# Kernel optimization log

Measured on AMD Instinct MI355X. Metric: run time of the kernel, lower is better.

## Reference

```python
import jax, jax.numpy as jnp
import numpy as np

B, S, D, H = 4, 2048, 1024, 16
HD = D // H
THETA = 10000.0


def rope(x, pos, theta=THETA):
    # x: [..., seq, d], pos: broadcastable to [..., seq]
    d = x.shape[-1]
    half = d // 2
    inv_freq = 1.0 / (theta ** (jnp.arange(half, dtype=jnp.float32) * 2.0 / d))  # [half]
    ang = pos[..., None].astype(jnp.float32) * inv_freq  # [..., seq, half]
    cos, sin = jnp.cos(ang), jnp.sin(ang)
    x1, x2 = x[..., 0::2], x[..., 1::2]
    r1 = x1 * cos - x2 * sin
    r2 = x1 * sin + x2 * cos
    return jnp.stack([r1, r2], axis=-1).reshape(x.shape).astype(x.dtype)


def setup_inputs() -> dict:
    key = jax.random.key(0)
    ks = jax.random.split(key, 5)
    x = jax.random.normal(ks[0], (B, S, D), dtype=jnp.float32)
    token_positions = jnp.tile(jnp.arange(S, dtype=jnp.int64 if jax.config.jax_enable_x64 else jnp.int32), (B, 1))
    scale = 0.02
    Wq = jax.random.normal(ks[1], (D, D), dtype=jnp.float32) * scale
    Wk = jax.random.normal(ks[2], (D, D), dtype=jnp.float32) * scale
    Wv = jax.random.normal(ks[3], (D, D), dtype=jnp.float32) * scale
    Wo = jax.random.normal(ks[4], (D, D), dtype=jnp.float32) * scale
    return {"x": x, "token_positions": token_positions, "Wq": Wq, "Wk": Wk, "Wv": Wv, "Wo": Wo}


def reference(x, token_positions, Wq, Wk, Wv, Wo):
    b, s, d = x.shape
    # QKV projections (torch Linear: x @ W.T), split heads -> [b, h, s, hd]
    def proj(W):
        y = jnp.einsum('bsd,ed->bse', x, W)
        return y.reshape(b, s, H, HD).transpose(0, 2, 1, 3)
    Q, K, V = proj(Wq), proj(Wk), proj(Wv)
    # token_positions [..., seq] -> [..., 1, seq] to broadcast over heads
    pos = token_positions[:, None, :]  # [b, 1, s]
    Q = rope(Q, pos)
    K = rope(K, pos)
    # causal mask and scaled dot-product attention
    idx = jnp.arange(s)
    causal = idx[:, None] >= idx[None, :]  # [s, s], query >= key
    scores = jnp.einsum('bhqd,bhkd->bhqk', Q, K) / jnp.sqrt(jnp.float32(HD))
    scores = jnp.where(causal, scores, -jnp.inf)
    weights = jax.nn.softmax(scores, axis=-1)
    o = jnp.einsum('bhqk,bhkd->bhqd', weights, V)
    o = o.transpose(0, 2, 1, 3).reshape(b, s, d)  # merge heads
    return jnp.einsum('bsd,ed->bse', o, Wo)
```

## Files before the change

### kernel.cpp

```cpp
#include <hip/hip_runtime.h>

#define S_LEN 2048
#define NH 16
#define HDIM 64
#define DMODEL 1024

typedef __attribute__((ext_vector_type(8))) short bf16x8;
typedef __attribute__((ext_vector_type(4))) float f32x4;

__device__ __forceinline__ short f2bf(float f) {
    union { float f; unsigned u; } x; x.f = f;
    unsigned r = x.u + 0x7fffu + ((x.u >> 16) & 1u);
    return (short)(r >> 16);
}

#define GLDS(g, l) __builtin_amdgcn_global_load_lds( \
    (__attribute__((address_space(1))) void*)(g),    \
    (__attribute__((address_space(3))) void*)(l), 16, 0, 0)

#define QSCALE 0.18033688011112042f
#define FREQ_L 0.41524101186109327f

__global__ __launch_bounds__(256) void prep(const float* __restrict__ x,
                                            const float* __restrict__ wq,
                                            const float* __restrict__ wk,
                                            const float* __restrict__ wv,
                                            const float* __restrict__ wo,
                                            const int* __restrict__ tp,
                                            short* __restrict__ xb,
                                            short* __restrict__ wqb,
                                            short* __restrict__ wkb,
                                            short* __restrict__ wvb,
                                            short* __restrict__ wob,
                                            float2* __restrict__ tab) {
    int bid = blockIdx.x;
    if (bid < 8192) {
        int i = bid * 256 + threadIdx.x;
        float4 v = ((const float4*)x)[i];
        short4 o;
        o.x = f2bf(v.x); o.y = f2bf(v.y); o.z = f2bf(v.z); o.w = f2bf(v.w);
        ((short4*)xb)[i] = o;
    } else if (bid < 12288) {
        int sel = (bid - 8192) >> 10;
        const float* in = sel == 0 ? wq : sel == 1 ? wk : sel == 2 ? wv : wo;
        short* out = sel == 0 ? wqb : sel == 1 ? wkb : sel == 2 ? wvb : wob;
        int i = ((bid - 8192) & 1023) * 256 + threadIdx.x;
        float4 v = ((const float4*)in)[i];
        short4 o;
        o.x = f2bf(v.x); o.y = f2bf(v.y); o.z = f2bf(v.z); o.w = f2bf(v.w);
        ((short4*)out)[i] = o;
    } else {
        int idx = (bid - 12288) * 256 + threadIdx.x;
        int b = idx >> 16, s = (idx >> 5) & 2047, i = idx & 31;
        float p = (float)tp[(b << 11) + s];
        float freq = exp2f(-(float)i * FREQ_L);
        float sn, cs;
        sincosf(p * freq, &sn, &cs);
        tab[idx] = make_float2(cs, sn);
    }
}

__global__ __launch_bounds__(256) void gemm_qkv(const short* __restrict__ A,
                                                const short* __restrict__ Bq,
                                                const short* __restrict__ Bk,
                                                const short* __restrict__ Bv,
                                                const float2* __restrict__ tab,
                                                short* __restrict__ Qo,
                                                short* __restrict__ Ko,
                                                short* __restrict__ Vo) {
    constexpr int K = 1024, BK = 64;
    __shared__ __align__(16) short smem[2 * 128 * BK];
    short* sa = smem;
    short* sb = smem + 128 * BK;

    const int sel = blockIdx.x >> 3;
    const int bn = blockIdx.x & 7;
    const int bm = blockIdx.y;
    const short* Bm = sel == 0 ? Bq : sel == 1 ? Bk : Bv;
    short* Cb = sel == 0 ? Qo : sel == 1 ? Ko : Vo;

    const int tid = threadIdx.x;
    const int lane = tid & 63;
    const int w = tid >> 6;
    const int wm = w >> 1, wn = w & 1;
    const int quad = lane >> 4, l16 = lane & 15;
    const int l7 = l16 & 7;

    int aoff[4], boff[4];
#pragma unroll
    for (int i = 0; i < 4; i++) {
        int Lc = i * 256 + tid;
        int row = Lc >> 3;
        int cc = (Lc & 7) ^ (row & 7);
        aoff[i] = (bm * 128 + row) * K + cc * 8;
        boff[i] = (bn * 128 + row) * K + cc * 8;
    }

    f32x4 acc[4][4] = {};

    for (int k0 = 0; k0 < K; k0 += BK) {
#pragma unroll
        for (int i = 0; i < 4; i++)
            GLDS(A + aoff[i] + k0, (char*)sa + i * 4096 + w * 1024);
#pragma unroll
        for (int i = 0; i < 4; i++)
            GLDS(Bm + boff[i] + k0, (char*)sb + i * 4096 + w * 1024);
        __syncthreads();

#pragma unroll
        for (int kc = 0; kc < 2; kc++) {
            const int c = ((kc * 4 + quad) ^ l7) * 8;
            bf16x8 af[4], bfm[4];
#pragma unroll
            for (int mi = 0; mi < 4; mi++)
                af[mi] = *(const bf16x8*)&sa[(wm * 64 + mi * 16 + l16) * BK + c];
#pragma unroll
            for (int ni = 0; ni < 4; ni++)
                bfm[ni] = *(const bf16x8*)&sb[(wn * 64 + ni * 16 + l16) * BK + c];
#pragma unroll
            for (int mi = 0; mi < 4; mi++)
#pragma unroll
                for (int ni = 0; ni < 4; ni++)
                    acc[mi][ni] = __builtin_amdgcn_mfma_f32_16x16x32_bf16(af[mi], bfm[ni],
                                                                          acc[mi][ni], 0, 0, 0);
        }
        __syncthreads();
    }

    const int gm0 = bm * 128 + wm * 64;
    const int gn0 = bn * 128 + wn * 64;

    if (sel == 2) {
        short* T = smem;
#pragma unroll
        for (int mi = 0; mi < 4; mi++) {
            int lmb = wm * 64 + mi * 16 + quad * 4;
#pragma unroll
            for (int ni = 0; ni < 4; ni++) {
                int ln = wn * 64 + ni * 16 + l16;
                short4 pk;
                pk.x = f2bf(acc[mi][ni][0]);
                pk.y = f2bf(acc[mi][ni][1]);
                pk.z = f2bf(acc[mi][ni][2]);
                pk.w = f2bf(acc[mi][ni][3]);
                *(short4*)&T[ln * 128 + (lmb ^ ((ln & 15) << 3))] = pk;
            }
        }
        __syncthreads();
        const int row = tid >> 1, half = tid & 1;
        const int grow = bn * 128 + row;
        const int gb = (bm * 128) >> 11;
        const int gs0 = (bm * 128) & 2047;
        short* dst = Cb + (((size_t)(gb * NH + (grow >> 6)) * HDIM + (grow & 63)) * S_LEN
                           + gs0 + half * 64);
#pragma unroll
        for (int j = 0; j < 8; j++) {
            bf16x8 v = *(const bf16x8*)&T[row * 128 +
                        ((half * 64 + j * 8) ^ ((row & 15) << 3))];
            *(bf16x8*)(dst + j * 8) = v;
        }
    } else {
        const float qs = (sel == 0) ? QSCALE : 1.0f;
#pragma unroll
        for (int mi = 0; mi < 4; mi++)
#pragma unroll
            for (int r = 0; r < 4; r++) {
                int gm = gm0 + mi * 16 + quad * 4 + r;
                const float2* trow = tab + (gm << 5);
                int b = gm >> 11, s = gm & 2047;
#pragma unroll
                for (int ni = 0; ni < 4; ni++) {
                    float2 cs = trow[ni * 8 + (l16 >> 1)];
                    float v = acc[mi][ni][r];
                    float prt = __shfl_xor(v, 1, 64);
                    float val = (l16 & 1) ? (prt * cs.y + v * cs.x)
                                          : (v * cs.x - prt * cs.y);
                    int gn = gn0 + ni * 16 + l16;
                    int h = gn >> 6, hd = gn & 63;
                    Cb[((b * NH + h) * S_LEN + s) * HDIM + hd] = f2bf(val * qs);
                }
            }
    }
}

__global__ __launch_bounds__(256) void gemm_o(const short* __restrict__ A,
                                              const short* __restrict__ Bw,
                                              float* __restrict__ Cf) {
    constexpr int N = 1024, K = 1024, BK = 32;
    __shared__ __align__(16) short sa[3][128 * BK];
    __shared__ __align__(16) short sb[3][64 * BK];

    const int tid = threadIdx.x;
    const int lane = tid & 63;
    const int w = tid >> 6;
    const int quad = lane >> 4, l16 = lane & 15;
    const int bn = blockIdx.x, bm = blockIdx.y;
    const int arow0 = bm * 128, brow0 = bn * 64;

    int aoff[2], boff;
#pragma unroll
    for (int i = 0; i < 2; i++) {
        int cs = i * 256 + tid;
        int row = cs >> 2;
        int gc = (cs & 3) ^ ((row >> 1) & 3);
        aoff[i] = (arow0 + row) * K + gc * 8;
    }
    {
        int row = tid >> 2;
        int gc = (tid & 3) ^ ((row >> 1) & 3);
        boff = (brow0 + row) * K + gc * 8;
    }

    auto stage = [&](int kt, int b) {
        const int k0 = kt * BK;
#pragma unroll
        for (int i = 0; i < 2; i++)
            GLDS(A + aoff[i] + k0, (char*)&sa[b][0] + i * 4096 + w * 1024);
        GLDS(Bw + boff + k0, (char*)&sb[b][0] + w * 1024);
    };

    f32x4 acc[2][4] = {};
    const int rsw = (quad ^ ((l16 >> 1) & 3)) * 8;

    auto compute = [&](int b) {
        bf16x8 af[2];
#pragma unroll
        for (int mi = 0; mi < 2; mi++)
            af[mi] = *(const bf16x8*)&sa[b][(w * 32 + mi * 16 + l16) * BK + rsw];
#pragma unroll
        for (int ni = 0; ni < 4; ni++) {
            bf16x8 bfr = *(const bf16x8*)&sb[b][(ni * 16 + l16) * BK + rsw];
#pragma unroll
            for (int mi = 0; mi < 2; mi++)
                acc[mi][ni] = __builtin_amdgcn_mfma_f32_16x16x32_bf16(af[mi], bfr,
                                                                     acc[mi][ni], 0, 0, 0);
        }
    };

    stage(0, 0);
    stage(1, 1);

    auto step = [&](int kt, int b, int bs) {
        asm volatile("s_waitcnt vmcnt(3)" ::: "memory");
        __builtin_amdgcn_s_barrier();
        __builtin_amdgcn_sched_barrier(0);
        stage(kt + 2, bs);
        compute(b);
    };

    for (int kt = 0; kt < 30; kt += 3) {
        step(kt + 0, 0, 2);
        step(kt + 1, 1, 0);
        step(kt + 2, 2, 1);
    }
    asm volatile("s_waitcnt vmcnt(3)" ::: "memory");
    __builtin_amdgcn_s_barrier();
    __builtin_amdgcn_sched_barrier(0);
    compute(0);
    asm volatile("s_waitcnt vmcnt(0)" ::: "memory");
    __builtin_amdgcn_s_barrier();
    __builtin_amdgcn_sched_barrier(0);
    compute(1);

    const int gm0 = arow0 + w * 32;
#pragma unroll
    for (int mi = 0; mi < 2; mi++)
#pragma unroll
        for (int ni = 0; ni < 4; ni++)
#pragma unroll
            for (int r = 0; r < 4; r++) {
                int gm = gm0 + mi * 16 + quad * 4 + r;
                int gn = brow0 + ni * 16 + l16;
                Cf[gm * N + gn] = acc[mi][ni][r];
            }
}

__global__ __launch_bounds__(256, 3) void attn(const short* __restrict__ Q,
                                               const short* __restrict__ Km,
                                               const short* __restrict__ Vt,
                                               short* __restrict__ O) {
    __shared__ __align__(16) short kbuf[2][64 * 64];
    __shared__ __align__(16) short vbuf[2][64 * 64];
    __shared__ __align__(16) short pbuf[4][32 * 64];

    const int lane = threadIdx.x & 63;
    const int w = threadIdx.x >> 6;
    const int quad = lane >> 4, l16 = lane & 15;
    const int l7 = l16 & 7;
    const int bh = blockIdx.y;

    const short* Qg = Q  + bh * S_LEN * 64;
    const short* Kg = Km + bh * S_LEN * 64;
    const short* Vg = Vt + bh * 64 * S_LEN;
    short* myp = &pbuf[w][0];

    const int b = bh >> 4, h = bh & 15;

    bf16x8 ones;
#pragma unroll
    for (int j = 0; j < 8; j++) ones[j] = (short)0x3f80;

    auto stage = [&](int kt, int par) {
        const short* kt_base = Kg + kt * 64 * 64;
        const short* vt_base = Vg + kt * 64;
#pragma unroll
        for (int i = 0; i < 2; ++i) {
            int ch = w * 128 + i * 64 + lane;
            int row = ch >> 3;
            int c = (ch & 7) ^ (row & 7);
            GLDS(kt_base + row * 64 + c * 8, (char*)&kbuf[par][(w * 128 + i * 64) * 8]);
        }
#pragma unroll
        for (int i = 0; i < 2; ++i) {
            int ch = w * 128 + i * 64 + lane;
            int row = ch >> 3;
            int c = (ch & 7) ^ (row & 7);
            GLDS(vt_base + row * S_LEN + c * 8, (char*)&vbuf[par][(w * 128 + i * 64) * 8]);
        }
    };

    const int QtA = blockIdx.x;
    const int QtB = 15 - blockIdx.x;

    stage(0, 0);
    int t = 0;

    for (int phase = 0; phase < 2; ++phase) {
        const int Qt = phase ? QtB : QtA;
        const int nkt = 2 * Qt + 2;

        bf16x8 aq[2][2];
#pragma unroll
        for (int mi = 0; mi < 2; mi++) {
            int qrow = Qt * 128 + w * 32 + mi * 16 + l16;
#pragma unroll
            for (int kc = 0; kc < 2; kc++)
                aq[mi][kc] = *(const bf16x8*)&Qg[qrow * 64 + kc * 32 + quad * 8];
        }

        f32x4 oacc[2][4] = {};
        f32x4 lacc[2] = {};

        for (int kt = 0; kt < nkt; ++kt, ++t) {
            __syncthreads();
            if (kt + 1 < nkt)    stage(kt + 1, (t + 1) & 1);
            else if (phase == 0) stage(0,      (t + 1) & 1);
            const short* kb_cur = &kbuf[t & 1][0];
            const short* vb_cur = &vbuf[t & 1][0];

            f32x4 sc[2][4] = {};
#pragma unroll
            for (int nt = 0; nt < 4; nt++) {
                int raddr = (nt * 16 + l16) * 64;
#pragma unroll
                for (int kc = 0; kc < 2; kc++) {
                    bf16x8 kf = *(const bf16x8*)&kb_cur[raddr + (((quad + kc * 4) ^ l7) * 8)];
                    sc[0][nt] = __builtin_amdgcn_mfma_f32_16x16x32_bf16(aq[0][kc], kf, sc[0][nt], 0, 0, 0);
                    sc[1][nt] = __builtin_amdgcn_mfma_f32_16x16x32_bf16(aq[1][kc], kf, sc[1][nt], 0, 0, 0);
                }
            }
            if (kt >= nkt - 2) {
#pragma unroll
                for (int mi = 0; mi < 2; mi++)
#pragma unroll
                    for (int nt = 0; nt < 4; nt++)
#pragma unroll
                        for (int r = 0; r < 4; r++) {
                            int col = kt * 64 + nt * 16 + l16;
                            int row = Qt * 128 + w * 32 + mi * 16 + quad * 4 + r;
                            if (col > row) sc[mi][nt][r] = -__builtin_inff();
                        }
            }
#pragma unroll
            for (int mi = 0; mi < 2; mi++)
#pragma unroll
                for (int nt = 0; nt < 4; nt++)
#pragma unroll
                    for (int r = 0; r < 4; r++) {
                        float pv = __builtin_amdgcn_exp2f(sc[mi][nt][r]);
                        int q = mi * 16 + quad * 4 + r;
                        union { float f; unsigned short us[2]; } uu;
                        uu.f = pv;
                        myp[q * 64 + (((nt * 2 + (l16 >> 3)) ^ (q & 7)) * 8) + l7] =
                            (short)uu.us[1];
                    }
            bf16x8 ap[2][2];
#pragma unroll
            for (int mi = 0; mi < 2; mi++)
#pragma unroll
                for (int kc = 0; kc < 2; kc++)
                    ap[mi][kc] = *(const bf16x8*)&myp[(mi * 16 + l16) * 64 +
                                                      (((quad + kc * 4) ^ l7) * 8)];
#pragma unroll
            for (int nt = 0; nt < 4; nt++) {
                int raddr = (nt * 16 + l16) * 64;
#pragma unroll
                for (int kc = 0; kc < 2; kc++) {
                    bf16x8 vf = *(const bf16x8*)&vb_cur[raddr + (((quad + kc * 4) ^ l7) * 8)];
                    oacc[0][nt] = __builtin_amdgcn_mfma_f32_16x16x32_bf16(ap[0][kc], vf, oacc[0][nt], 0, 0, 0);
                    oacc[1][nt] = __builtin_amdgcn_mfma_f32_16x16x32_bf16(ap[1][kc], vf, oacc[1][nt], 0, 0, 0);
                }
            }
#pragma unroll
            for (int mi = 0; mi < 2; mi++) {
                lacc[mi] = __builtin_amdgcn_mfma_f32_16x16x32_bf16(ap[mi][0], ones, lacc[mi], 0, 0, 0);
                lacc[mi] = __builtin_amdgcn_mfma_f32_16x16x32_bf16(ap[mi][1], ones, lacc[mi], 0, 0, 0);
            }
        }
#pragma unroll
        for (int mi = 0; mi < 2; mi++)
#pragma unroll
            for (int r = 0; r < 4; r++) {
                float inv = 1.0f / lacc[mi][r];
                int srow = Qt * 128 + w * 32 + mi * 16 + quad * 4 + r;
#pragma unroll
                for (int nt = 0; nt < 4; nt++) {
                    int hd = nt * 16 + l16;
                    O[(b * S_LEN + srow) * DMODEL + h * HDIM + hd] = f2bf(oacc[mi][nt][r] * inv);
                }
            }
    }
}

extern "C" void kernel_launch(void* const* d_in, const int* in_sizes, int n_in,
                              void* d_out, int out_size, void* d_ws, size_t ws_size,
                              hipStream_t stream) {
    const float* x  = (const float*)d_in[0];
    const int*   tp = (const int*)d_in[1];
    const float* Wq = (const float*)d_in[2];
    const float* Wk = (const float*)d_in[3];
    const float* Wv = (const float*)d_in[4];
    const float* Wo = (const float*)d_in[5];
    float* out = (float*)d_out;

    char* ws = (char*)d_ws;
    const size_t MB = 1024 * 1024;
    short* xb  = (short*)(ws);
    short* wqb = (short*)(ws + 16 * MB);
    short* wkb = (short*)(ws + 18 * MB);
    short* wvb = (short*)(ws + 20 * MB);
    short* wob = (short*)(ws + 22 * MB);
    short* Qb  = (short*)(ws + 24 * MB);
    short* Kb  = (short*)(ws + 40 * MB);
    short* Vtb = (short*)(ws + 56 * MB);
    float2* tab = (float2*)d_out;

    prep<<<13312, 256, 0, stream>>>(x, Wq, Wk, Wv, Wo, tp,
                                    xb, wqb, wkb, wvb, wob, tab);

    gemm_qkv<<<dim3(24, 64), 256, 0, stream>>>(xb, wqb, wkb, wvb, tab, Qb, Kb, Vtb);

    attn<<<dim3(8, 64), 256, 0, stream>>>(Qb, Kb, Vtb, xb);

    gemm_o<<<dim3(16, 64), 256, 0, stream>>>(xb, wob, out);
}
```

Baseline: 263.6 us.

## Pipeline QKV GEMM with 4-stage async LDS ring and 256x128 tiles

Rewrites the QKV projection GEMM to use 512-thread blocks computing 256x128 tiles, which halves the grid in M. The K loop now runs in 32-wide slices through a 4-slot LDS ring buffer that keeps three loads in flight, waits on vmcnt and issues a single barrier per step. The MFMA section also raises wave priority. The aim is to hide global-to-LDS latency and increase reuse of the B tile. The cost is 96KB of LDS per block, fewer blocks, and more delicate synchronisation.

```diff
diff --git a/kernel.cpp b/kernel.cpp
--- a/kernel.cpp
+++ b/kernel.cpp
@@ -60,7 +60,7 @@
     }
 }
 
-__global__ __launch_bounds__(256) void gemm_qkv(const short* __restrict__ A,
+__global__ __launch_bounds__(512) void gemm_qkv(const short* __restrict__ A,
                                                 const short* __restrict__ Bq,
                                                 const short* __restrict__ Bk,
                                                 const short* __restrict__ Bv,
@@ -68,10 +68,8 @@
                                                 short* __restrict__ Qo,
                                                 short* __restrict__ Ko,
                                                 short* __restrict__ Vo) {
-    constexpr int K = 1024, BK = 64;
-    __shared__ __align__(16) short smem[2 * 128 * BK];
-    short* sa = smem;
-    short* sb = smem + 128 * BK;
+    constexpr int K = 1024;
+    __shared__ __align__(16) short smem[4 * 12288];
 
     const int sel = blockIdx.x >> 3;
     const int bn = blockIdx.x & 7;
@@ -82,56 +80,84 @@
     const int tid = threadIdx.x;
     const int lane = tid & 63;
     const int w = tid >> 6;
-    const int wm = w >> 1, wn = w & 1;
+    const int wm = w >> 1;
+    const int wn = w & 1;
     const int quad = lane >> 4, l16 = lane & 15;
-    const int l7 = l16 & 7;
-
-    int aoff[4], boff[4];
-#pragma unroll
-    for (int i = 0; i < 4; i++) {
-        int Lc = i * 256 + tid;
-        int row = Lc >> 3;
-        int cc = (Lc & 7) ^ (row & 7);
-        aoff[i] = (bm * 128 + row) * K + cc * 8;
-        boff[i] = (bn * 128 + row) * K + cc * 8;
-    }
+
+    int aoff[2], boffv;
+#pragma unroll
+    for (int i = 0; i < 2; i++) {
+        int Lc = i * 512 + tid;
+        int row = Lc >> 2;
+        int gc = (Lc & 3) ^ (row & 3);
+        aoff[i] = (bm * 256 + row) * K + gc * 8;
+    }
+    {
+        int row = tid >> 2;
+        int gc = (tid & 3) ^ (row & 3);
+        boffv = (bn * 128 + row) * K + gc * 8;
+    }
+
+    auto stage = [&](int h) {
+        char* slotB = (char*)smem + (h & 3) * 24576;
+        const int kh = h * 32;
+#pragma unroll
+        for (int i = 0; i < 2; i++)
+            GLDS(A + aoff[i] + kh, slotB + i * 8192 + w * 1024);
+        GLDS(Bm + boffv + kh, slotB + 16384 + w * 1024);
+    };
 
     f32x4 acc[4][4] = {};
-
-    for (int k0 = 0; k0 < K; k0 += BK) {
-#pragma unroll
-        for (int i = 0; i < 4; i++)
-            GLDS(A + aoff[i] + k0, (char*)sa + i * 4096 + w * 1024);
-#pragma unroll
-        for (int i = 0; i < 4; i++)
-            GLDS(Bm + boff[i] + k0, (char*)sb + i * 4096 + w * 1024);
-        __syncthreads();
-
-#pragma unroll
-        for (int kc = 0; kc < 2; kc++) {
-            const int c = ((kc * 4 + quad) ^ l7) * 8;
-            bf16x8 af[4], bfm[4];
-#pragma unroll
-            for (int mi = 0; mi < 4; mi++)
-                af[mi] = *(const bf16x8*)&sa[(wm * 64 + mi * 16 + l16) * BK + c];
+    const int rsw = (quad ^ (l16 & 3)) * 8;
+
+    auto compute = [&](int h) {
+        const short* sA = smem + (h & 3) * 12288;
+        const short* sB = sA + 8192;
+        bf16x8 af[4], bfm[4];
+#pragma unroll
+        for (int mi = 0; mi < 4; mi++)
+            af[mi] = *(const bf16x8*)&sA[(wm * 64 + mi * 16 + l16) * 32 + rsw];
+#pragma unroll
+        for (int ni = 0; ni < 4; ni++)
+            bfm[ni] = *(const bf16x8*)&sB[(wn * 64 + ni * 16 + l16) * 32 + rsw];
+        __builtin_amdgcn_s_setprio(1);
+#pragma unroll
+        for (int mi = 0; mi < 4; mi++)
 #pragma unroll
             for (int ni = 0; ni < 4; ni++)
-                bfm[ni] = *(const bf16x8*)&sb[(wn * 64 + ni * 16 + l16) * BK + c];
-#pragma unroll
-            for (int mi = 0; mi < 4; mi++)
-#pragma unroll
-                for (int ni = 0; ni < 4; ni++)
-                    acc[mi][ni] = __builtin_amdgcn_mfma_f32_16x16x32_bf16(af[mi], bfm[ni],
-                                                                          acc[mi][ni], 0, 0, 0);
-        }
-        __syncthreads();
-    }
-
-    const int gm0 = bm * 128 + wm * 64;
+                acc[mi][ni] = __builtin_amdgcn_mfma_f32_16x16x32_bf16(af[mi], bfm[ni],
+                                                                      acc[mi][ni], 0, 0, 0);
+        __builtin_amdgcn_s_setprio(0);
+    };
+
+    stage(0); stage(1); stage(2);
+
+    for (int h = 0; h < 29; ++h) {
+        asm volatile("s_waitcnt vmcnt(6)" ::: "memory");
+        __builtin_amdgcn_s_barrier();
+        __builtin_amdgcn_sched_barrier(0);
+        stage(h + 3);
+        compute(h);
+    }
+    asm volatile("s_waitcnt vmcnt(6)" ::: "memory");
+    __builtin_amdgcn_s_barrier();
+    __builtin_amdgcn_sched_barrier(0);
+    compute(29);
+    asm volatile("s_waitcnt vmcnt(3)" ::: "memory");
+    __builtin_amdgcn_s_barrier();
+    __builtin_amdgcn_sched_barrier(0);
+    compute(30);
+    asm volatile("s_waitcnt vmcnt(0)" ::: "memory");
+    __builtin_amdgcn_s_barrier();
+    __builtin_amdgcn_sched_barrier(0);
+    compute(31);
+
+    const int gm0 = bm * 256 + wm * 64;
     const int gn0 = bn * 128 + wn * 64;
 
     if (sel == 2) {
         short* T = smem;
+        __syncthreads();
 #pragma unroll
         for (int mi = 0; mi < 4; mi++) {
             int lmb = wm * 64 + mi * 16 + quad * 4;
@@ -143,20 +169,20 @@
                 pk.y = f2bf(acc[mi][ni][1]);
                 pk.z = f2bf(acc[mi][ni][2]);
                 pk.w = f2bf(acc[mi][ni][3]);
-                *(short4*)&T[ln * 128 + (lmb ^ ((ln & 15) << 3))] = pk;
+                *(short4*)&T[ln * 256 + (lmb ^ ((ln & 31) << 3))] = pk;
             }
         }
         __syncthreads();
-        const int row = tid >> 1, half = tid & 1;
+        const int row = tid >> 2, qt = tid & 3;
         const int grow = bn * 128 + row;
-        const int gb = (bm * 128) >> 11;
-        const int gs0 = (bm * 128) & 2047;
+        const int gb = bm >> 3;
+        const int gs0 = (bm & 7) * 256;
         short* dst = Cb + (((size_t)(gb * NH + (grow >> 6)) * HDIM + (grow & 63)) * S_LEN
-                           + gs0 + half * 64);
+                           + gs0 + qt * 64);
 #pragma unroll
         for (int j = 0; j < 8; j++) {
-            bf16x8 v = *(const bf16x8*)&T[row * 128 +
-                        ((half * 64 + j * 8) ^ ((row & 15) << 3))];
+            bf16x8 v = *(const bf16x8*)&T[row * 256 +
+                        ((qt * 64 + j * 8) ^ ((row & 31) << 3))];
             *(bf16x8*)(dst + j * 8) = v;
         }
     } else {
@@ -448,7 +474,7 @@
     prep<<<13312, 256, 0, stream>>>(x, Wq, Wk, Wv, Wo, tp,
                                     xb, wqb, wkb, wvb, wob, tab);
 
-    gemm_qkv<<<dim3(24, 64), 256, 0, stream>>>(xb, wqb, wkb, wvb, tab, Qb, Kb, Vtb);
+    gemm_qkv<<<dim3(24, 32), 512, 0, stream>>>(xb, wqb, wkb, wvb, tab, Qb, Kb, Vtb);
 
     attn<<<dim3(8, 64), 256, 0, stream>>>(Qb, Kb, Vtb, xb);
 
```

Measured after the change: 262.9 us. Within noise of the previous version (-0.2%).
